# Optimization experiments

Hardware: AMD Instinct MI355X
Metric: run time of the kernel (lower is better)

## Reference

```python
import jax, jax.numpy as jnp
import numpy as np

EMB_DIM = 256
N_EMBED = 1024
BETA = 0.25


def setup_inputs() -> dict:
    key = jax.random.key(0)
    k1, k2 = jax.random.split(key)
    encoderout = jax.random.normal(k1, (32, EMB_DIM, 32, 32), dtype=jnp.float32)
    # embedding.weight.data.normal_(mean=0, std=1/n_embed)
    codebook = jax.random.normal(k2, (N_EMBED, EMB_DIM), dtype=jnp.float32) * (1.0 / N_EMBED)
    return {"encoderout": encoderout, "codebook": codebook}


def reference(encoderout, codebook):
    # NCHW -> NHWC
    x = jnp.transpose(encoderout, (0, 2, 3, 1))  # [B,H,W,D]
    flat = x.reshape(-1, EMB_DIM)                # [N,D]
    d2 = (jnp.sum(flat * flat, axis=1, keepdims=True)
          + jnp.sum(codebook * codebook, axis=1)[None, :]
          - 2.0 * flat @ codebook.T)             # [N,K]
    idx = jnp.argmin(d2, axis=1)                 # [N]
    quant = codebook[idx].reshape(x.shape)       # [B,H,W,D]
    codebook_loss = jnp.mean((quant - jax.lax.stop_gradient(x)) ** 2)
    commitment_loss = jnp.mean((x - jax.lax.stop_gradient(quant)) ** 2)
    loss = codebook_loss + BETA * commitment_loss
    # FAITHFUL to source bug: straight-through output is overwritten by the
    # input permuted back to NCHW, so out == encoderout.
    out = jnp.transpose(x, (0, 3, 1, 2))
    return (out, loss, codebook_loss, commitment_loss)
```

## Files before the change

### kernel.cpp

```cpp
#include <hip/hip_runtime.h>
#include <stdint.h>


#define EMB 256
#define ELEMS 8388608
#define NBLK 512

typedef __bf16 bf16x8 __attribute__((ext_vector_type(8)));
typedef float  f32x4  __attribute__((ext_vector_type(4)));

union Frag { uint4 u4; bf16x8 v; };

__device__ __forceinline__ unsigned short f2bf(float f) {
    unsigned u = __float_as_uint(f);
    u += 0x7FFFu + ((u >> 16) & 1u);
    return (unsigned short)(u >> 16);
}

__global__ __launch_bounds__(256) void vq_prep(const float* __restrict__ cb,
                                               uint2* __restrict__ cbswz,
                                               float* __restrict__ esq,
                                               float* __restrict__ accum,
                                               unsigned* __restrict__ done) {
    if (blockIdx.x == 0 && threadIdx.x == 0) { accum[0] = 0.f; done[0] = 0u; }

    const int tid  = threadIdx.x;
    const int w    = tid >> 6;
    const int lane = tid & 63;
    const int n    = blockIdx.x * 4 + w;

    const float4* row = (const float4*)(cb + n * EMB);
    float4 v = row[lane];

    float s = v.x * v.x + v.y * v.y + v.z * v.z + v.w * v.w;
    #pragma unroll
    for (int m = 1; m <= 32; m <<= 1) s += __shfl_xor(s, m);
    if (lane == 0) esq[n] = s;

    unsigned lo = (unsigned)f2bf(v.x) | ((unsigned)f2bf(v.y) << 16);
    unsigned hi = (unsigned)f2bf(v.z) | ((unsigned)f2bf(v.w) << 16);
    int kc = lane >> 1;
    int h  = lane & 1;
    cbswz[n * 64 + ((kc ^ (n & 7)) << 1) + h] = make_uint2(lo, hi);
}


#define STAGE(nc_, dst_) do {                                                  \
    const char* _src = cbbase + (size_t)(nc_) * 32768;                         \
    _Pragma("unroll")                                                          \
    for (int _i = 0; _i < 8; ++_i) {                                           \
        const int _o = (_i * 4 + w) * 1024;         \
        __builtin_amdgcn_global_load_lds(                                      \
            (const __attribute__((address_space(1))) unsigned int*)            \
                (_src + _o + lane * 16),                                       \
            (__attribute__((address_space(3))) unsigned int*)                  \
                ((char*)(dst_) + _o),                                          \
            16, 0, 0);                                                         \
    } } while (0)

#define CHUNK(nc_, buf_) do {                                                  \
    f32x4 _a0 = (f32x4){0.f,0.f,0.f,0.f};                                      \
    f32x4 _a1 = (f32x4){0.f,0.f,0.f,0.f};                                      \
    f32x4 _a2 = (f32x4){0.f,0.f,0.f,0.f};                                      \
    f32x4 _a3 = (f32x4){0.f,0.f,0.f,0.f};                                      \
    _Pragma("unroll")                                                          \
    for (int _ks = 0; _ks < 8; ++_ks) {                                        \
        Frag _fb; _fb.u4 = (buf_)[nl * 32 + ((_ks * 4 + q) ^ (nl & 7))];       \
        _a0 = __builtin_amdgcn_mfma_f32_16x16x32_bf16(afr[0][_ks], _fb.v, _a0, 0, 0, 0); \
        _a1 = __builtin_amdgcn_mfma_f32_16x16x32_bf16(afr[1][_ks], _fb.v, _a1, 0, 0, 0); \
        _a2 = __builtin_amdgcn_mfma_f32_16x16x32_bf16(afr[2][_ks], _fb.v, _a2, 0, 0, 0); \
        _a3 = __builtin_amdgcn_mfma_f32_16x16x32_bf16(afr[3][_ks], _fb.v, _a3, 0, 0, 0); \
    }                                                                          \
    const float _eq = esq[(nc_) * 64 + nl];                                    \
    _Pragma("unroll")                                                          \
    for (int _r2 = 0; _r2 < 4; ++_r2) {                                        \
        rmin[0][_r2] = fminf(rmin[0][_r2], fmaf(-2.f, _a0[_r2], _eq));         \
        rmin[1][_r2] = fminf(rmin[1][_r2], fmaf(-2.f, _a1[_r2], _eq));         \
        rmin[2][_r2] = fminf(rmin[2][_r2], fmaf(-2.f, _a2[_r2], _eq));         \
        rmin[3][_r2] = fminf(rmin[3][_r2], fmaf(-2.f, _a3[_r2], _eq));         \
    } } while (0)

__global__ __launch_bounds__(256, 2) void vq_main(const float* __restrict__ enc,
                                                  const uint4* __restrict__ cbswz,
                                                  const float* __restrict__ esq,
                                                  float* __restrict__ out,
                                                  float* __restrict__ accum,
                                                  unsigned* __restrict__ done) {
    __shared__ uint4 As[2048];
    __shared__ uint4 Bs[2048];
    __shared__ float dmin[4][64];
    __shared__ float partsA[4];

    const int tid  = threadIdx.x;
    const int w    = tid >> 6;
    const int lane = tid & 63;
    const int q    = lane >> 4;
    const int c    = lane & 15;

    const int b   = blockIdx.x >> 4;
    const int hw0 = (blockIdx.x & 15) << 6;
    const float* encB = enc + (size_t)b * 262144 + hw0;
    float*       outB = out + (size_t)b * 262144 + hw0;
    const char* cbbase = (const char*)cbswz;

    const int q4 = tid & 15;
    const int kg = tid >> 4;
    float sx = 0.f;
    {
        f32x4 vh[16];
        #pragma unroll
        for (int j = 0; j < 16; ++j)
            vh[j] = __builtin_nontemporal_load(
                (const f32x4*)(encB + (size_t)(kg * 16 + j) * 1024 + q4 * 4));
        #pragma unroll
        for (int j = 0; j < 16; ++j) {
            __builtin_nontemporal_store(vh[j],
                (f32x4*)(outB + (size_t)(kg * 16 + j) * 1024 + q4 * 4));
            #pragma unroll
            for (int i2 = 0; i2 < 4; ++i2) sx = fmaf(vh[j][i2], vh[j][i2], sx);
        }
        #pragma unroll
        for (int i = 0; i < 4; ++i) {
            unsigned short us[16];
            #pragma unroll
            for (int j = 0; j < 16; ++j) us[j] = f2bf(vh[j][i]);
            uint4 pk0, pk1;
            pk0.x = (unsigned)us[0]  | ((unsigned)us[1]  << 16);
            pk0.y = (unsigned)us[2]  | ((unsigned)us[3]  << 16);
            pk0.z = (unsigned)us[4]  | ((unsigned)us[5]  << 16);
            pk0.w = (unsigned)us[6]  | ((unsigned)us[7]  << 16);
            pk1.x = (unsigned)us[8]  | ((unsigned)us[9]  << 16);
            pk1.y = (unsigned)us[10] | ((unsigned)us[11] << 16);
            pk1.z = (unsigned)us[12] | ((unsigned)us[13] << 16);
            pk1.w = (unsigned)us[14] | ((unsigned)us[15] << 16);
            const int r = q4 * 4 + i;
            As[r * 32 + ((2 * kg + 0) ^ (r & 7))] = pk0;
            As[r * 32 + ((2 * kg + 1) ^ (r & 7))] = pk1;
        }
    }
    #pragma unroll
    for (int m = 1; m <= 32; m <<= 1) sx += __shfl_xor(sx, m);
    if (lane == 0) partsA[w] = sx;
    __syncthreads();

    bf16x8 afr[4][8];
    #pragma unroll
    for (int mi = 0; mi < 4; ++mi) {
        const int r = mi * 16 + c;
        #pragma unroll
        for (int ks = 0; ks < 8; ++ks) {
            Frag fa; fa.u4 = As[r * 32 + ((ks * 4 + q) ^ (r & 7))];
            afr[mi][ks] = fa.v;
        }
    }

    float rmin[4][4];
    #pragma unroll
    for (int mi = 0; mi < 4; ++mi)
        #pragma unroll
        for (int r2 = 0; r2 < 4; ++r2) rmin[mi][r2] = 1e30f;

    const int nl = w * 16 + c;

    __syncthreads();
    STAGE(0, As);

    for (int i = 0; i < 8; ++i) {
        __syncthreads();
        STAGE(2 * i + 1, Bs);
        CHUNK(2 * i, (const uint4*)As);
        __syncthreads();
        if (i < 7) STAGE(2 * i + 2, As);
        CHUNK(2 * i + 1, (const uint4*)Bs);
    }

    #pragma unroll
    for (int mi = 0; mi < 4; ++mi)
        #pragma unroll
        for (int r2 = 0; r2 < 4; ++r2) {
            float x = rmin[mi][r2];
            x = fminf(x, __shfl_xor(x, 1));
            x = fminf(x, __shfl_xor(x, 2));
            x = fminf(x, __shfl_xor(x, 4));
            x = fminf(x, __shfl_xor(x, 8));
            rmin[mi][r2] = x;
        }
    if (c == 0) {
        #pragma unroll
        for (int mi = 0; mi < 4; ++mi)
            #pragma unroll
            for (int r2 = 0; r2 < 4; ++r2)
                dmin[w][mi * 16 + q * 4 + r2] = rmin[mi][r2];
    }
    __syncthreads();

    if (tid < 64) {
        float vr = fminf(fminf(dmin[0][tid], dmin[1][tid]),
                         fminf(dmin[2][tid], dmin[3][tid]));
        #pragma unroll
        for (int m = 1; m <= 32; m <<= 1) vr += __shfl_xor(vr, m);
        if (tid == 0) {
            float s = vr + partsA[0] + partsA[1] + partsA[2] + partsA[3];
            atomicAdd(accum, s);
            __threadfence();
            unsigned prev = atomicAdd(done, 1u);
            if (prev == NBLK - 1) {
                float tot = atomicAdd(accum, 0.0f);
                float cbl = tot * (1.0f / (float)ELEMS);
                out[ELEMS + 0] = 1.25f * cbl;
                out[ELEMS + 1] = cbl;
                out[ELEMS + 2] = cbl;
            }
        }
    }
}

extern "C" void kernel_launch(void* const* d_in, const int* in_sizes, int n_in,
                              void* d_out, int out_size, void* d_ws, size_t ws_size,
                              hipStream_t stream) {
    const float* enc = (const float*)d_in[0];
    const float* cb  = (const float*)d_in[1];
    float* out = (float*)d_out;

    float*    accum = (float*)d_ws;
    unsigned* done  = (unsigned*)((char*)d_ws + 64);
    float*    esq   = (float*)((char*)d_ws + 256);
    uint2*    cbswz = (uint2*)((char*)d_ws + 8192);

    vq_prep<<<dim3(256), dim3(256), 0, stream>>>(cb, cbswz, esq, accum, done);
    vq_main<<<dim3(NBLK), dim3(256), 0, stream>>>(enc, (const uint4*)cbswz, esq,
                                                  out, accum, done);
}
```

Baseline: 115.3 us.

## Load codebook fragments directly into registers instead of staging through LDS

The codebook is re-laid out in the prep kernel so that each lane's MFMA B fragment for every chunk sits at a contiguous, coalesced global address. The main kernel then loads these fragments straight into registers, prefetching the next chunk while the current chunk's MFMAs run. This removes the LDS double buffer, the global_load_lds staging and the per-chunk barriers. In exchange every block reads the codebook from global/L2 per lane, register pressure goes up, and each load has less time to hide its latency.

```diff
diff --git a/kernel.cpp b/kernel.cpp
--- a/kernel.cpp
+++ b/kernel.cpp
@@ -39,37 +39,32 @@
 
     unsigned lo = (unsigned)f2bf(v.x) | ((unsigned)f2bf(v.y) << 16);
     unsigned hi = (unsigned)f2bf(v.z) | ((unsigned)f2bf(v.w) << 16);
-    int kc = lane >> 1;
-    int h  = lane & 1;
-    cbswz[n * 64 + ((kc ^ (n & 7)) << 1) + h] = make_uint2(lo, hi);
-}
-
-
-#define STAGE(nc_, dst_) do {                                                  \
-    const char* _src = cbbase + (size_t)(nc_) * 32768;                         \
-    _Pragma("unroll")                                                          \
-    for (int _i = 0; _i < 8; ++_i) {                                           \
-        const int _o = (_i * 4 + w) * 1024;         \
-        __builtin_amdgcn_global_load_lds(                                      \
-            (const __attribute__((address_space(1))) unsigned int*)            \
-                (_src + _o + lane * 16),                                       \
-            (__attribute__((address_space(3))) unsigned int*)                  \
-                ((char*)(dst_) + _o),                                          \
-            16, 0, 0);                                                         \
-    } } while (0)
-
-#define CHUNK(nc_, buf_) do {                                                  \
+    const int kc = lane >> 1;
+    const int h  = lane & 1;
+    const unsigned idx4 = ((unsigned)(n >> 6) << 11) + ((unsigned)(kc >> 2) << 8)
+                        + ((unsigned)(n & 63) << 2) + (unsigned)(kc & 3);
+    cbswz[idx4 * 2 + h] = make_uint2(lo, hi);
+}
+
+
+#define MFMA4(ks_) do {                                                        \
+    bf16x8 _bv = bfr[ks_].v;                                                   \
+    _a0 = __builtin_amdgcn_mfma_f32_16x16x32_bf16(afr[0][ks_], _bv, _a0, 0, 0, 0); \
+    _a1 = __builtin_amdgcn_mfma_f32_16x16x32_bf16(afr[1][ks_], _bv, _a1, 0, 0, 0); \
+    _a2 = __builtin_amdgcn_mfma_f32_16x16x32_bf16(afr[2][ks_], _bv, _a2, 0, 0, 0); \
+    _a3 = __builtin_amdgcn_mfma_f32_16x16x32_bf16(afr[3][ks_], _bv, _a3, 0, 0, 0); \
+} while (0)
+
+#define CHUNK_BODY(nc_, LOADNEXT_) do {                                        \
     f32x4 _a0 = (f32x4){0.f,0.f,0.f,0.f};                                      \
     f32x4 _a1 = (f32x4){0.f,0.f,0.f,0.f};                                      \
     f32x4 _a2 = (f32x4){0.f,0.f,0.f,0.f};                                      \
     f32x4 _a3 = (f32x4){0.f,0.f,0.f,0.f};                                      \
     _Pragma("unroll")                                                          \
     for (int _ks = 0; _ks < 8; ++_ks) {                                        \
-        Frag _fb; _fb.u4 = (buf_)[nl * 32 + ((_ks * 4 + q) ^ (nl & 7))];       \
-        _a0 = __builtin_amdgcn_mfma_f32_16x16x32_bf16(afr[0][_ks], _fb.v, _a0, 0, 0, 0); \
-        _a1 = __builtin_amdgcn_mfma_f32_16x16x32_bf16(afr[1][_ks], _fb.v, _a1, 0, 0, 0); \
-        _a2 = __builtin_amdgcn_mfma_f32_16x16x32_bf16(afr[2][_ks], _fb.v, _a2, 0, 0, 0); \
-        _a3 = __builtin_amdgcn_mfma_f32_16x16x32_bf16(afr[3][_ks], _fb.v, _a3, 0, 0, 0); \
+        MFMA4(_ks);                                                            \
+        if (LOADNEXT_)       \
+            bfr[_ks].u4 = pc[((nc_) + 1) * 2048 + _ks * 256];                  \
     }                                                                          \
     const float _eq = esq[(nc_) * 64 + nl];                                    \
     _Pragma("unroll")                                                          \
@@ -87,7 +82,6 @@
                                                   float* __restrict__ accum,
                                                   unsigned* __restrict__ done) {
     __shared__ uint4 As[2048];
-    __shared__ uint4 Bs[2048];
     __shared__ float dmin[4][64];
     __shared__ float partsA[4];
 
@@ -101,7 +95,9 @@
     const int hw0 = (blockIdx.x & 15) << 6;
     const float* encB = enc + (size_t)b * 262144 + hw0;
     float*       outB = out + (size_t)b * 262144 + hw0;
-    const char* cbbase = (const char*)cbswz;
+
+    const int nl = w * 16 + c;
+    const uint4* pc = cbswz + (size_t)(nl * 4 + q);
 
     const int q4 = tid & 15;
     const int kg = tid >> 4;
@@ -138,6 +134,11 @@
             As[r * 32 + ((2 * kg + 1) ^ (r & 7))] = pk1;
         }
     }
+
+    Frag bfr[8];
+    #pragma unroll
+    for (int ks = 0; ks < 8; ++ks) bfr[ks].u4 = pc[ks * 256];
+
     #pragma unroll
     for (int m = 1; m <= 32; m <<= 1) sx += __shfl_xor(sx, m);
     if (lane == 0) partsA[w] = sx;
@@ -160,19 +161,8 @@
         #pragma unroll
         for (int r2 = 0; r2 < 4; ++r2) rmin[mi][r2] = 1e30f;
 
-    const int nl = w * 16 + c;
-
-    __syncthreads();
-    STAGE(0, As);
-
-    for (int i = 0; i < 8; ++i) {
-        __syncthreads();
-        STAGE(2 * i + 1, Bs);
-        CHUNK(2 * i, (const uint4*)As);
-        __syncthreads();
-        if (i < 7) STAGE(2 * i + 2, As);
-        CHUNK(2 * i + 1, (const uint4*)Bs);
-    }
+    for (int nc = 0; nc < 15; ++nc) CHUNK_BODY(nc, 1);
+    CHUNK_BODY(15, 0);
 
     #pragma unroll
     for (int mi = 0; mi < 4; ++mi)
```

Result: no change. 116.2 us (+0.8%).
